# Kernel optimization log

Measured on AMD Instinct MI355X. Metric: run time of the kernel, lower is better.

Reference implementation:

```python
import jax, jax.numpy as jnp
import numpy as np

B, N, C = 2, 4096, 1024
H, WIN = 16, 20
D = C // H

def setup_inputs() -> dict:
    key = jax.random.key(0)
    ks = jax.random.split(key, 9)
    s = 1.0 / np.sqrt(C)
    d = {"q": jax.random.normal(ks[0], (B, N, C), jnp.float32)}
    for i, name in enumerate(["Wq", "Wk", "Wv", "Wo"]):
        d[name + "_w"] = jax.random.normal(ks[1 + 2 * i], (C, C), jnp.float32) * s
        d[name + "_b"] = jax.random.normal(ks[2 + 2 * i], (C,), jnp.float32) * 0.01
    return d

def reference(q, Wq_w, Wq_b, Wk_w, Wk_b, Wv_w, Wv_b, Wo_w, Wo_b):
    b, n, c = q.shape
    w2 = WIN // 2  # half window = 10
    def proj(x, w, bias):
        return (x @ w.T + bias).reshape(b, n, H, D).transpose(0, 2, 1, 3)  # [B,H,N,D]
    Q = proj(q, Wq_w, Wq_b)
    K = proj(q, Wk_w, Wk_b)
    V = proj(q, Wv_w, Wv_b)
    off = jnp.arange(-w2, w2 + 1)                       # [Wn] = 21 offsets
    pos = jnp.arange(n)[:, None] + off[None, :]         # [N, Wn] key index per query
    valid = (pos >= 0) & (pos < n)                      # edge clipping == torch start/end slicing
    idx = jnp.clip(pos, 0, n - 1)
    Kw = K[:, :, idx, :]                                # [B,H,N,Wn,D] gathered key windows
    Vw = V[:, :, idx, :]
    scale = jnp.sqrt(jnp.float32(D))
    scores = jnp.einsum('bhnd,bhnwd->bhnw', Q, Kw) / scale
    scores = jnp.where(valid[None, None], scores, -jnp.inf)
    probs = jax.nn.softmax(scores, axis=-1)             # invalid slots get exactly 0
    out = jnp.einsum('bhnw,bhnwd->bhnd', probs, Vw)
    out = out.transpose(0, 2, 1, 3).reshape(b, n, c)
    out = out @ Wo_w.T + Wo_b
    # torch returns attn_probs of the LAST loop iteration i=N-1: window [N-1-w2, N), size w2+1
    attn_last = probs[:, :, -1:, : w2 + 1]              # [B,H,1,11]
    return (out, attn_last)
```

## Files before the change

kernel.cpp:

```cpp
#include <hip/hip_runtime.h>
#include <hip/hip_bf16.h>

#define Bb 2
#define Nn 4096
#define Cc 1024
#define Hh 16
#define Dd 64
#define Mm (Bb*Nn)
#define W2 10
#define WINSZ 21

typedef __attribute__((ext_vector_type(8))) short  bf16x8s;
typedef __attribute__((ext_vector_type(4))) float  f32x4;
typedef __attribute__((ext_vector_type(4))) unsigned short us4;

#define AS1 __attribute__((address_space(1)))
#define AS3 __attribute__((address_space(3)))

__device__ __forceinline__ unsigned short f2bf(float f) {
  unsigned int u = __float_as_uint(f);
  u += 0x7FFFu + ((u >> 16) & 1u);
  return (unsigned short)(u >> 16);
}
__device__ __forceinline__ float bflo(unsigned int u) { return __uint_as_float(u << 16); }
__device__ __forceinline__ float bfhi(unsigned int u) { return __uint_as_float(u & 0xFFFF0000u); }

__device__ __forceinline__ us4 cvt4(float4 v) {
  us4 o;
  o.x = f2bf(v.x); o.y = f2bf(v.y); o.z = f2bf(v.z); o.w = f2bf(v.w);
  return o;
}

__global__ __launch_bounds__(256) void cvt_all(const float4* __restrict__ q,
                                               const float4* __restrict__ wq,
                                               const float4* __restrict__ wk,
                                               const float4* __restrict__ wv,
                                               const float4* __restrict__ wo,
                                               const float* __restrict__ bq,
                                               const float* __restrict__ bk,
                                               const float* __restrict__ bv,
                                               us4* __restrict__ qb4,
                                               us4* __restrict__ wqkv4,
                                               us4* __restrict__ wo4,
                                               float* __restrict__ bqkv) {
  const int NQ = 2097152, NW = 262144, TOT = NQ + 4 * NW;
  const int gid = blockIdx.x * 256 + threadIdx.x;
  const int stride = gridDim.x * 256;
  for (int i = gid; i < TOT; i += stride) {
    if (i < NQ) {
      qb4[i] = cvt4(q[i]);
    } else {
      int j = i - NQ;
      int r = j >> 18, k = j & (NW - 1);
      if (r == 0)      wqkv4[k]          = cvt4(wq[k]);
      else if (r == 1) wqkv4[NW + k]     = cvt4(wk[k]);
      else if (r == 2) wqkv4[2 * NW + k] = cvt4(wv[k]);
      else             wo4[k]            = cvt4(wo[k]);
    }
  }
  if (gid < 3072) {
    float v = (gid < 1024) ? bq[gid] : (gid < 2048) ? bk[gid - 1024] : bv[gid - 2048];
    bqkv[gid] = v;
  }
}

template<bool OUT_BF16>
__global__ __launch_bounds__(512) void gemm_p3(const unsigned short* __restrict__ A,
                                               const unsigned short* __restrict__ Bm,
                                               const float* __restrict__ bias,
                                               void* __restrict__ Cout,
                                               int N) {
  constexpr int K = 1024, NT = 16, NBM = Mm / 128;
  __shared__ unsigned short lds[3][24576];

  const int tid = threadIdx.x, wid = tid >> 6, lane = tid & 63;
  const int wm = wid >> 2, wn = wid & 3;

  const int nwg = gridDim.x, cpx = nwg >> 3, bid = blockIdx.x;
  const int swz = (bid & 7) * cpx + (bid >> 3);
  const int m0 = (swz % NBM) << 7, n0 = (swz / NBM) << 8;

  const int rbase = wid * 8 + (lane >> 3);
  const int cst = ((lane & 7) ^ (lane >> 3)) * 8;
  const unsigned short* aS0 = A + (size_t)(m0 + rbase) * K + cst;
  const unsigned short* aS1 = A + (size_t)(m0 + 64 + rbase) * K + cst;
  const unsigned short* bS0 = Bm + (size_t)(n0 + rbase) * K + cst;
  const unsigned short* bS1 = Bm + (size_t)(n0 + 64 + rbase) * K + cst;
  const unsigned short* bS2 = Bm + (size_t)(n0 + 128 + rbase) * K + cst;
  const unsigned short* bS3 = Bm + (size_t)(n0 + 192 + rbase) * K + cst;
  const int dA0 = wid * 512, dA1 = 4096 + wid * 512;
  const int dB0 = 8192 + wid * 512, dB1 = 12288 + wid * 512;
  const int dB2 = 16384 + wid * 512, dB3 = 20480 + wid * 512;

#define STG(bf, kt) do {                                                                   \
    const size_t ko = (size_t)(kt) * 64;                                                   \
    __builtin_amdgcn_global_load_lds((AS1 const void*)(aS0 + ko), (AS3 void*)(&lds[bf][dA0]), 16, 0, 0); \
    __builtin_amdgcn_global_load_lds((AS1 const void*)(aS1 + ko), (AS3 void*)(&lds[bf][dA1]), 16, 0, 0); \
    __builtin_amdgcn_global_load_lds((AS1 const void*)(bS0 + ko), (AS3 void*)(&lds[bf][dB0]), 16, 0, 0); \
    __builtin_amdgcn_global_load_lds((AS1 const void*)(bS1 + ko), (AS3 void*)(&lds[bf][dB1]), 16, 0, 0); \
    __builtin_amdgcn_global_load_lds((AS1 const void*)(bS2 + ko), (AS3 void*)(&lds[bf][dB2]), 16, 0, 0); \
    __builtin_amdgcn_global_load_lds((AS1 const void*)(bS3 + ko), (AS3 void*)(&lds[bf][dB3]), 16, 0, 0); \
  } while (0)

  int aoff[2][4], boff[2][4];
#pragma unroll
  for (int kk = 0; kk < 2; ++kk) {
    const int chs = ((kk * 4 + (lane >> 4)) ^ (lane & 7)) * 8;
#pragma unroll
    for (int f = 0; f < 4; ++f) {
      aoff[kk][f] = (wm * 64 + f * 16 + (lane & 15)) * 64 + chs;
      boff[kk][f] = 8192 + (wn * 64 + f * 16 + (lane & 15)) * 64 + chs;
    }
  }

  f32x4 acc[4][4] = {};

  STG(0, 0);
  STG(1, 1);
  asm volatile("s_waitcnt vmcnt(6)" ::: "memory");
  __builtin_amdgcn_sched_barrier(0);
  __builtin_amdgcn_s_barrier();
  __builtin_amdgcn_sched_barrier(0);

  int cur = 0, stg = 2;
  for (int t = 0; t < NT; ++t) {
    if (t + 2 < NT) STG(stg, t + 2);

    const unsigned short* L = &lds[cur][0];
    bf16x8s a[2][4], b[2][4];
#pragma unroll
    for (int kk = 0; kk < 2; ++kk) {
#pragma unroll
      for (int f = 0; f < 4; ++f) {
        a[kk][f] = *(const bf16x8s*)(L + aoff[kk][f]);
        b[kk][f] = *(const bf16x8s*)(L + boff[kk][f]);
      }
    }
    __builtin_amdgcn_s_setprio(1);
#pragma unroll
    for (int kk = 0; kk < 2; ++kk)
#pragma unroll
      for (int fm = 0; fm < 4; ++fm)
#pragma unroll
        for (int fn = 0; fn < 4; ++fn)
          acc[fm][fn] = __builtin_amdgcn_mfma_f32_16x16x32_bf16(a[kk][fm], b[kk][fn], acc[fm][fn], 0, 0, 0);
    __builtin_amdgcn_s_setprio(0);

    if (t + 1 < NT) {
      if (t + 2 < NT) asm volatile("s_waitcnt vmcnt(6)" ::: "memory");
      else            asm volatile("s_waitcnt vmcnt(0)" ::: "memory");
      __builtin_amdgcn_sched_barrier(0);
      __builtin_amdgcn_s_barrier();
      __builtin_amdgcn_sched_barrier(0);
    }
    cur = (cur == 2) ? 0 : cur + 1;
    stg = (stg == 2) ? 0 : stg + 1;
  }
#undef STG

  const int r0 = m0 + wm * 64 + (lane >> 4) * 4;
  const int c0 = n0 + wn * 64 + (lane & 15);
#pragma unroll
  for (int fm = 0; fm < 4; ++fm) {
#pragma unroll
    for (int fn = 0; fn < 4; ++fn) {
      const int col = c0 + fn * 16;
      const float bv = bias[col];
#pragma unroll
      for (int r = 0; r < 4; ++r) {
        const int row = r0 + fm * 16 + r;
        const float v = acc[fm][fn][r] + bv;
        if (OUT_BF16)
          ((unsigned short*)Cout)[(size_t)row * N + col] = f2bf(v);
        else
          ((float*)Cout)[(size_t)row * N + col] = v;
      }
    }
  }
}

#define TN 128
#define KVROWS (TN + 2 * W2)

__global__ void attn_kernel(const unsigned short* __restrict__ QKV,
                            unsigned short* __restrict__ AO,
                            float* __restrict__ attn_last) {
  __shared__ uint4 Kl[KVROWS * 8];
  __shared__ uint4 Vl[KVROWS * 8];

  const int nt = Nn / TN;
  const int bid = blockIdx.x;
  const int tile = bid & (nt - 1);
  const int bh = bid / nt;
  const int h = bh & (Hh - 1), b = bh / Hh;
  const int n0 = tile * TN;
  const int tid = threadIdx.x;

  for (int idx = tid; idx < KVROWS * 8; idx += 256) {
    const int r = idx >> 3, c = idx & 7;
    const int pos = n0 - W2 + r;
    uint4 kv = make_uint4(0, 0, 0, 0), vv = make_uint4(0, 0, 0, 0);
    if (pos >= 0 && pos < Nn) {
      const uint4* row = (const uint4*)(QKV + (size_t)(b * Nn + pos) * 3072);
      kv = row[128 + h * 8 + c];
      vv = row[256 + h * 8 + c];
    }
    const int slot = c ^ (r & 7);
    Kl[r * 8 + slot] = kv;
    Vl[r * 8 + slot] = vv;
  }
  __syncthreads();

  const int row  = tid >> 1;
  const int half = tid & 1;
  const int n = n0 + row;
  const size_t m = (size_t)b * Nn + n;

  const uint4* qrow = (const uint4*)(QKV + m * 3072) + h * 8 + half * 4;
  const uint4 qd0 = qrow[0], qd1 = qrow[1], qd2 = qrow[2], qd3 = qrow[3];

  float p[WINSZ];
#pragma unroll
  for (int w = 0; w < WINSZ; ++w) p[w] = 0.f;

#pragma unroll
  for (int c = 0; c < 4; ++c) {
    const uint4 qv = (c == 0) ? qd0 : (c == 1) ? qd1 : (c == 2) ? qd2 : qd3;
    const float q0 = bflo(qv.x), q1 = bfhi(qv.x);
    const float q2 = bflo(qv.y), q3 = bfhi(qv.y);
    const float q4 = bflo(qv.z), q5 = bfhi(qv.z);
    const float q6 = bflo(qv.w), q7 = bfhi(qv.w);
#pragma unroll 7
    for (int w = 0; w < WINSZ; ++w) {
      const int r = row + w;
      const uint4 v = Kl[r * 8 + ((half * 4 + c) ^ (r & 7))];
      float a0 = q0 * bflo(v.x);
      float a1 = q1 * bfhi(v.x);
      a0 += q2 * bflo(v.y);
      a1 += q3 * bfhi(v.y);
      a0 += q4 * bflo(v.z);
      a1 += q5 * bfhi(v.z);
      a0 += q6 * bflo(v.w);
      a1 += q7 * bfhi(v.w);
      p[w] += a0 + a1;
    }
  }

#pragma unroll
  for (int w = 0; w < WINSZ; ++w) {
    float t = p[w];
    t += __shfl_xor(t, 1, 64);
    const int pos = n - W2 + w;
    p[w] = (pos < 0 || pos >= Nn) ? -1e30f : t * 0.125f;
  }
  float mx = p[0];
#pragma unroll
  for (int w = 1; w < WINSZ; ++w) mx = fmaxf(mx, p[w]);
  float sum = 0.f;
#pragma unroll
  for (int w = 0; w < WINSZ; ++w) { p[w] = __expf(p[w] - mx); sum += p[w]; }
  const float inv = 1.0f / sum;

  if (n == Nn - 1 && half == 0) {
#pragma unroll
    for (int w = 0; w <= W2; ++w)
      attn_last[(b * Hh + h) * (W2 + 1) + w] = p[w] * inv;
  }

  uint4* orow = (uint4*)(AO + m * Cc + h * Dd) + half * 4;
#pragma unroll
  for (int c = 0; c < 4; ++c) {
    float o0 = 0.f, o1 = 0.f, o2 = 0.f, o3 = 0.f;
    float o4 = 0.f, o5 = 0.f, o6 = 0.f, o7 = 0.f;
#pragma unroll 7
    for (int w = 0; w < WINSZ; ++w) {
      const int r = row + w;
      const uint4 v = Vl[r * 8 + ((half * 4 + c) ^ (r & 7))];
      const float pw = p[w];
      o0 += pw * bflo(v.x);
      o1 += pw * bfhi(v.x);
      o2 += pw * bflo(v.y);
      o3 += pw * bfhi(v.y);
      o4 += pw * bflo(v.z);
      o5 += pw * bfhi(v.z);
      o6 += pw * bflo(v.w);
      o7 += pw * bfhi(v.w);
    }
    unsigned int d0 = (unsigned int)f2bf(o0 * inv) | ((unsigned int)f2bf(o1 * inv) << 16);
    unsigned int d1 = (unsigned int)f2bf(o2 * inv) | ((unsigned int)f2bf(o3 * inv) << 16);
    unsigned int d2 = (unsigned int)f2bf(o4 * inv) | ((unsigned int)f2bf(o5 * inv) << 16);
    unsigned int d3 = (unsigned int)f2bf(o6 * inv) | ((unsigned int)f2bf(o7 * inv) << 16);
    orow[c] = make_uint4(d0, d1, d2, d3);
  }
}

extern "C" void kernel_launch(void* const* d_in, const int* in_sizes, int n_in,
                              void* d_out, int out_size, void* d_ws, size_t ws_size,
                              hipStream_t stream) {
  const float* q    = (const float*)d_in[0];
  const float* Wq_w = (const float*)d_in[1];
  const float* Wq_b = (const float*)d_in[2];
  const float* Wk_w = (const float*)d_in[3];
  const float* Wk_b = (const float*)d_in[4];
  const float* Wv_w = (const float*)d_in[5];
  const float* Wv_b = (const float*)d_in[6];
  const float* Wo_w = (const float*)d_in[7];
  const float* Wo_b = (const float*)d_in[8];
  float* out = (float*)d_out;
  float* attn_last = out + (size_t)Mm * Cc;

  char* ws = (char*)d_ws;
  unsigned short* qb   = (unsigned short*)(ws);
  unsigned short* Wqkv = (unsigned short*)(ws + 16777216);
  unsigned short* Wo16 = (unsigned short*)(ws + 16777216 + 6291456);
  float*          bqkv = (float*)(ws + 25165824);
  unsigned short* QKV  = (unsigned short*)(ws + 25182208);
  unsigned short* AO   = (unsigned short*)(ws + 75513856);

  cvt_all<<<2048, 256, 0, stream>>>((const float4*)q,
                                    (const float4*)Wq_w, (const float4*)Wk_w,
                                    (const float4*)Wv_w, (const float4*)Wo_w,
                                    Wq_b, Wk_b, Wv_b,
                                    (us4*)qb, (us4*)Wqkv, (us4*)Wo16, bqkv);

  {
    dim3 grid((Mm / 128) * (3072 / 256));
    gemm_p3<true><<<grid, 512, 0, stream>>>(qb, Wqkv, bqkv, (void*)QKV, 3072);
  }

  {
    dim3 grid(Bb * Hh * (Nn / TN));
    attn_kernel<<<grid, 256, 0, stream>>>(QKV, AO, attn_last);
  }

  {
    dim3 grid((Mm / 128) * (Cc / 256));
    gemm_p3<false><<<grid, 512, 0, stream>>>(AO, Wo16, Wo_b, (void*)out, Cc);
  }
}
```

Measured before the change: 134.5 us.

## Use 256x256-tile GEMM with K-step 32 for QKV projection

Adds a new GEMM kernel with 256x256 output tiles and 32-wide K slices, triple-buffered via global_load_lds, each warp computing 128x64 with 8x4 MFMA fragments. It replaces the 128x256 tile kernel for the QKV projection, raising arithmetic intensity per LDS byte and halving the number of workgroups. In exchange it uses more accumulator registers (128 floats per lane) and has fewer blocks (384) for the CU count, which may hurt occupancy and wave balance.

Measured after the change: 141.1 us. 4.9% more time.

```diff
diff --git a/kernel.cpp b/kernel.cpp
--- a/kernel.cpp
+++ b/kernel.cpp
@@ -65,12 +65,116 @@
 }
 
 template<bool OUT_BF16>
+__global__ __launch_bounds__(512) void gemm_b256(const unsigned short* __restrict__ A,
+                                                 const unsigned short* __restrict__ Bm,
+                                                 const float* __restrict__ bias,
+                                                 void* __restrict__ Cout,
+                                                 int N) {
+  constexpr int K = 1024, NT = 32;
+  __shared__ unsigned short lds[3][16384];
+
+  const int tid = threadIdx.x, wid = tid >> 6, lane = tid & 63;
+  const int wm = wid >> 2, wn = wid & 3;
+
+  const int nwg = gridDim.x, cpx = nwg >> 3, bid = blockIdx.x;
+  const int swz = (bid & 7) * cpx + (bid >> 3);
+  constexpr int NBM = Mm / 256;
+  const int m0 = (swz % NBM) << 8, n0 = (swz / NBM) << 8;
+
+  const int srow = lane >> 2;
+  const int g8 = ((lane & 3) ^ ((lane >> 3) & 3)) * 8;
+  const unsigned short* aS0 = A  + (size_t)(m0 + wid * 32 + srow) * K + g8;
+  const unsigned short* aS1 = aS0 + (size_t)16 * K;
+  const unsigned short* bS0 = Bm + (size_t)(n0 + wid * 32 + srow) * K + g8;
+  const unsigned short* bS1 = bS0 + (size_t)16 * K;
+  const int dA0 = wid * 1024, dA1 = wid * 1024 + 512;
+  const int dB0 = 8192 + wid * 1024, dB1 = 8192 + wid * 1024 + 512;
+
+#define STG(bf, kt) do {                                                                    \
+    const size_t ko = (size_t)(kt) * 32;                                                    \
+    __builtin_amdgcn_global_load_lds((AS1 const void*)(aS0 + ko), (AS3 void*)(&lds[bf][dA0]), 16, 0, 0); \
+    __builtin_amdgcn_global_load_lds((AS1 const void*)(aS1 + ko), (AS3 void*)(&lds[bf][dA1]), 16, 0, 0); \
+    __builtin_amdgcn_global_load_lds((AS1 const void*)(bS0 + ko), (AS3 void*)(&lds[bf][dB0]), 16, 0, 0); \
+    __builtin_amdgcn_global_load_lds((AS1 const void*)(bS1 + ko), (AS3 void*)(&lds[bf][dB1]), 16, 0, 0); \
+  } while (0)
+
+  const int slot8 = ((lane >> 4) ^ (((lane & 15) >> 1) & 3)) * 8;
+  int aoff[8], boff[4];
+#pragma unroll
+  for (int f = 0; f < 8; ++f)
+    aoff[f] = (wm * 128 + f * 16 + (lane & 15)) * 32 + slot8;
+#pragma unroll
+  for (int f = 0; f < 4; ++f)
+    boff[f] = 8192 + (wn * 64 + f * 16 + (lane & 15)) * 32 + slot8;
+
+  f32x4 acc[8][4] = {};
+
+  STG(0, 0);
+  STG(1, 1);
+  asm volatile("s_waitcnt vmcnt(4)" ::: "memory");
+  __builtin_amdgcn_sched_barrier(0);
+  __builtin_amdgcn_s_barrier();
+  __builtin_amdgcn_sched_barrier(0);
+
+  int cur = 0, stg = 2;
+#pragma unroll 1
+  for (int t = 0; t < NT; ++t) {
+    if (t + 2 < NT) STG(stg, t + 2);
+
+    const unsigned short* L = &lds[cur][0];
+    bf16x8s a[8], b[4];
+#pragma unroll
+    for (int f = 0; f < 8; ++f) a[f] = *(const bf16x8s*)(L + aoff[f]);
+#pragma unroll
+    for (int f = 0; f < 4; ++f) b[f] = *(const bf16x8s*)(L + boff[f]);
+    __builtin_amdgcn_s_setprio(1);
+#pragma unroll
+    for (int fm = 0; fm < 8; ++fm)
+#pragma unroll
+      for (int fn = 0; fn < 4; ++fn)
+        acc[fm][fn] = __builtin_amdgcn_mfma_f32_16x16x32_bf16(a[fm], b[fn], acc[fm][fn], 0, 0, 0);
+    __builtin_amdgcn_s_setprio(0);
+
+    if (t + 1 < NT) {
+      if (t + 2 < NT) asm volatile("s_waitcnt vmcnt(4)" ::: "memory");
+      else            asm volatile("s_waitcnt vmcnt(0)" ::: "memory");
+      __builtin_amdgcn_sched_barrier(0);
+      __builtin_amdgcn_s_barrier();
+      __builtin_amdgcn_sched_barrier(0);
+    }
+    cur = (cur == 2) ? 0 : cur + 1;
+    stg = (stg == 2) ? 0 : stg + 1;
+  }
+#undef STG
+
+  const int r0 = m0 + wm * 128 + (lane >> 4) * 4;
+  const int c0 = n0 + wn * 64 + (lane & 15);
+#pragma unroll
+  for (int fm = 0; fm < 8; ++fm) {
+#pragma unroll
+    for (int fn = 0; fn < 4; ++fn) {
+      const int col = c0 + fn * 16;
+      const float bv = bias[col];
+#pragma unroll
+      for (int r = 0; r < 4; ++r) {
+        const int row = r0 + fm * 16 + r;
+        const float v = acc[fm][fn][r] + bv;
+        if (OUT_BF16)
+          ((unsigned short*)Cout)[(size_t)row * N + col] = f2bf(v);
+        else
+          ((float*)Cout)[(size_t)row * N + col] = v;
+      }
+    }
+  }
+}
+
+template<bool OUT_BF16>
 __global__ __launch_bounds__(512) void gemm_p3(const unsigned short* __restrict__ A,
                                                const unsigned short* __restrict__ Bm,
                                                const float* __restrict__ bias,
                                                void* __restrict__ Cout,
                                                int N) {
-  constexpr int K = 1024, NT = 16, NBM = Mm / 128;
+  constexpr int K = 1024, NT = 16;
   __shared__ unsigned short lds[3][24576];
 
   const int tid = threadIdx.x, wid = tid >> 6, lane = tid & 63;
@@ -78,6 +182,7 @@
 
   const int nwg = gridDim.x, cpx = nwg >> 3, bid = blockIdx.x;
   const int swz = (bid & 7) * cpx + (bid >> 3);
+  constexpr int NBM = Mm / 128;
   const int m0 = (swz % NBM) << 7, n0 = (swz / NBM) << 8;
 
   const int rbase = wid * 8 + (lane >> 3);
@@ -324,8 +429,8 @@
                                     (us4*)qb, (us4*)Wqkv, (us4*)Wo16, bqkv);
 
   {
-    dim3 grid((Mm / 128) * (3072 / 256));
-    gemm_p3<true><<<grid, 512, 0, stream>>>(qb, Wqkv, bqkv, (void*)QKV, 3072);
+    dim3 grid((Mm / 256) * (3072 / 256));
+    gemm_b256<true><<<grid, 512, 0, stream>>>(qb, Wqkv, bqkv, (void*)QKV, 3072);
   }
 
   {
```

## Use 256x256-tile ping-pong GEMM with setprio for QKV projection

Applied to the files above, without the earlier changes.

Adds a new GEMM kernel using 256x256 output tiles, double-buffered LDS (128KB), and a phased schedule. In that schedule MFMA blocks are wrapped in s_setprio and interleaved with LDS reads and global_load_lds staging of the next k-tiles. It replaces the 128x256 triple-buffered kernel for the QKV projection only. The larger tile raises data reuse per loaded byte, and the fine-grained interleave aims to overlap loads with math. The cost is more barriers, heavy register use (32 accumulators), and fewer workgroups (384), which may hurt occupancy and tail balance.

Result: slower. 137.5 us (+2.3%).

```diff
diff --git a/kernel.cpp b/kernel.cpp
--- a/kernel.cpp
+++ b/kernel.cpp
@@ -65,12 +65,122 @@
 }
 
 template<bool OUT_BF16>
+__global__ __launch_bounds__(512) void gemm8p(const unsigned short* __restrict__ A,
+                                              const unsigned short* __restrict__ Bm,
+                                              const float* __restrict__ bias,
+                                              void* __restrict__ Cout,
+                                              int N) {
+  constexpr int K = 1024;
+  __shared__ unsigned short lds[65536];
+
+  const int tid = threadIdx.x, wid = tid >> 6, lane = tid & 63;
+  const int wm = wid >> 2, wn = wid & 3;
+
+  const int nwg = gridDim.x, cpx = nwg >> 3, bid = blockIdx.x;
+  const int swz = (bid & 7) * cpx + (bid >> 3);
+  constexpr int NBM = Mm / 256;
+  const int m0 = (swz % NBM) << 8, n0 = (swz / NBM) << 8;
+
+  const int rbase = wid * 8 + (lane >> 3);
+  const int cst = ((lane & 7) ^ (lane >> 3)) * 8;
+  const unsigned short* aP0 = A  + (size_t)(m0 + rbase) * K + cst;
+  const unsigned short* aP1 = aP0 + (size_t)128 * K;
+  const unsigned short* bP0 = Bm + (size_t)(n0 + rbase) * K + cst;
+  const unsigned short* bP1 = bP0 + (size_t)128 * K;
+
+  const int awb = wm * 8192 + (lane & 15) * 64;
+  const int bwb = 16384 + (wn >> 1) * 8192 + (wn & 1) * 4096 + (lane & 15) * 64;
+  const int chs0 = (((lane >> 4)) ^ (lane & 7)) * 8;
+  const int chs1 = ((4 + (lane >> 4)) ^ (lane & 7)) * 8;
+
+  f32x4 acc[8][4] = {};
+  bf16x8s breg[4][2], areg[2][2];
+
+#define GL(sp, off) __builtin_amdgcn_global_load_lds((AS1 const void*)(sp), (AS3 void*)(&lds[off]), 16, 0, 0)
+#define STGA(d,h,kt) do { const unsigned short* _s = ((h) ? aP1 : aP0) + (size_t)(kt) * 64; \
+    GL(_s,                   (d)*32768 + (h)*8192 +        wid*512); \
+    GL(_s + (size_t)64 * K,  (d)*32768 + (h)*8192 + 4096 + wid*512); } while (0)
+#define STGB(d,h,kt) do { const unsigned short* _s = ((h) ? bP1 : bP0) + (size_t)(kt) * 64; \
+    GL(_s,                   (d)*32768 + 16384 + (h)*8192 +        wid*512); \
+    GL(_s + (size_t)64 * K,  (d)*32768 + 16384 + (h)*8192 + 4096 + wid*512); } while (0)
+#define LDB(d) do { _Pragma("unroll") for (int fn = 0; fn < 4; ++fn) { \
+    breg[fn][0] = *(const bf16x8s*)(&lds[(d)*32768 + bwb + fn*1024 + chs0]); \
+    breg[fn][1] = *(const bf16x8s*)(&lds[(d)*32768 + bwb + fn*1024 + chs1]); } } while (0)
+#define LDA(d,q) do { _Pragma("unroll") for (int u = 0; u < 2; ++u) { \
+    areg[u][0] = *(const bf16x8s*)(&lds[(d)*32768 + awb + ((q)*2+u)*1024 + chs0]); \
+    areg[u][1] = *(const bf16x8s*)(&lds[(d)*32768 + awb + ((q)*2+u)*1024 + chs1]); } } while (0)
+#define MF16(q) do { _Pragma("unroll") for (int u = 0; u < 2; ++u) _Pragma("unroll") for (int fn = 0; fn < 4; ++fn) { \
+    acc[(q)*2+u][fn] = __builtin_amdgcn_mfma_f32_16x16x32_bf16(areg[u][0], breg[fn][0], acc[(q)*2+u][fn], 0, 0, 0); \
+    acc[(q)*2+u][fn] = __builtin_amdgcn_mfma_f32_16x16x32_bf16(areg[u][1], breg[fn][1], acc[(q)*2+u][fn], 0, 0, 0); } } while (0)
+#define BAR __builtin_amdgcn_s_barrier()
+#define LGKM0 asm volatile("s_waitcnt lgkmcnt(0)" ::: "memory")
+#define PRIO1 __builtin_amdgcn_s_setprio(1)
+#define PRIO0 __builtin_amdgcn_s_setprio(0)
+
+  STGA(0,0,0); STGA(0,1,0); STGB(0,0,0); STGB(0,1,0);
+  STGA(1,0,1); STGA(1,1,1); STGB(1,0,1); STGB(1,1,1);
+  asm volatile("s_waitcnt vmcnt(8)" ::: "memory");
+  BAR;
+
+#pragma unroll 1
+  for (int j = 0; j < 8; ++j) {
+    const int tA1 = 2*j + 1;
+    const int t0  = (2*j + 2) & 15;
+    const int tB1 = (2*j + 3) & 15;
+    LDB(0); LDA(0,0); STGA(1,0,tA1);          BAR; LGKM0;
+    PRIO1; MF16(0); PRIO0; BAR;
+    LDA(0,1); STGA(1,1,tA1); STGB(0,0,t0);    BAR; LGKM0;
+    PRIO1; MF16(1); PRIO0; BAR;
+    LDA(0,2); STGB(0,1,t0);                   BAR; LGKM0;
+    PRIO1; MF16(2); PRIO0; BAR;
+    LDA(0,3);                                 BAR; LGKM0;
+    PRIO1; MF16(3); PRIO0;
+    asm volatile("s_waitcnt vmcnt(4)" ::: "memory"); BAR;
+    LDB(1); LDA(1,0); STGA(0,0,t0);           BAR; LGKM0;
+    PRIO1; MF16(0); PRIO0; BAR;
+    LDA(1,1); STGA(0,1,t0); STGB(1,0,tB1);    BAR; LGKM0;
+    PRIO1; MF16(1); PRIO0; BAR;
+    LDA(1,2); STGB(1,1,tB1);                  BAR; LGKM0;
+    PRIO1; MF16(2); PRIO0; BAR;
+    LDA(1,3);                                 BAR; LGKM0;
+    PRIO1; MF16(3); PRIO0;
+    asm volatile("s_waitcnt vmcnt(4)" ::: "memory"); BAR;
+  }
+#undef GL
+#undef STGA
+#undef STGB
+#undef LDB
+#undef LDA
+#undef MF16
+
+  const int r0 = m0 + wm * 128 + (lane >> 4) * 4;
+  const int c0 = n0 + wn * 64 + (lane & 15);
+#pragma unroll
+  for (int fm = 0; fm < 8; ++fm) {
+#pragma unroll
+    for (int fn = 0; fn < 4; ++fn) {
+      const int col = c0 + fn * 16;
+      const float bv = bias[col];
+#pragma unroll
+      for (int r = 0; r < 4; ++r) {
+        const int row = r0 + fm * 16 + r;
+        const float v = acc[fm][fn][r] + bv;
+        if (OUT_BF16)
+          ((unsigned short*)Cout)[(size_t)row * N + col] = f2bf(v);
+        else
+          ((float*)Cout)[(size_t)row * N + col] = v;
+      }
+    }
+  }
+}
+
+template<bool OUT_BF16>
 __global__ __launch_bounds__(512) void gemm_p3(const unsigned short* __restrict__ A,
                                                const unsigned short* __restrict__ Bm,
                                                const float* __restrict__ bias,
                                                void* __restrict__ Cout,
                                                int N) {
-  constexpr int K = 1024, NT = 16, NBM = Mm / 128;
+  constexpr int K = 1024, NT = 16;
   __shared__ unsigned short lds[3][24576];
 
   const int tid = threadIdx.x, wid = tid >> 6, lane = tid & 63;
@@ -78,6 +188,7 @@
 
   const int nwg = gridDim.x, cpx = nwg >> 3, bid = blockIdx.x;
   const int swz = (bid & 7) * cpx + (bid >> 3);
+  constexpr int NBM = Mm / 128;
   const int m0 = (swz % NBM) << 7, n0 = (swz / NBM) << 8;
 
   const int rbase = wid * 8 + (lane >> 3);
@@ -324,8 +435,8 @@
                                     (us4*)qb, (us4*)Wqkv, (us4*)Wo16, bqkv);
 
   {
-    dim3 grid((Mm / 128) * (3072 / 256));
-    gemm_p3<true><<<grid, 512, 0, stream>>>(qb, Wqkv, bqkv, (void*)QKV, 3072);
+    dim3 grid((Mm / 256) * (3072 / 256));
+    gemm8p<true><<<grid, 512, 0, stream>>>(qb, Wqkv, bqkv, (void*)QKV, 3072);
   }
 
   {
```

## Load GEMM B operand directly from global into registers, double-buffered

Applied to the files above, without the earlier changes.

The GEMM kernel no longer stages the weight (B) tile through LDS. Each wave loads its own B fragments straight from global memory into a double-buffered register set, prefetching the next k-step while the current one computes. A still goes through the 3-stage LDS ring, whose size drops from 24576 to 8192 shorts per stage, and the vmcnt waits are retuned. The aim is less LDS traffic and footprint and higher occupancy, at the cost of more VGPRs and uncoalesced, redundant global reads of B across the waves that share a column block.

New measurement: 212.7 us. 1.58x slower.

```diff
diff --git a/kernel.cpp b/kernel.cpp
--- a/kernel.cpp
+++ b/kernel.cpp
@@ -65,77 +65,76 @@
 }
 
 template<bool OUT_BF16>
-__global__ __launch_bounds__(512) void gemm_p3(const unsigned short* __restrict__ A,
+__global__ __launch_bounds__(512) void gemm_bd(const unsigned short* __restrict__ A,
                                                const unsigned short* __restrict__ Bm,
                                                const float* __restrict__ bias,
                                                void* __restrict__ Cout,
                                                int N) {
-  constexpr int K = 1024, NT = 16, NBM = Mm / 128;
-  __shared__ unsigned short lds[3][24576];
+  constexpr int K = 1024, NT = 16;
+  __shared__ unsigned short lds[3][8192];
 
   const int tid = threadIdx.x, wid = tid >> 6, lane = tid & 63;
   const int wm = wid >> 2, wn = wid & 3;
 
   const int nwg = gridDim.x, cpx = nwg >> 3, bid = blockIdx.x;
   const int swz = (bid & 7) * cpx + (bid >> 3);
+  constexpr int NBM = Mm / 128;
   const int m0 = (swz % NBM) << 7, n0 = (swz / NBM) << 8;
 
   const int rbase = wid * 8 + (lane >> 3);
   const int cst = ((lane & 7) ^ (lane >> 3)) * 8;
   const unsigned short* aS0 = A + (size_t)(m0 + rbase) * K + cst;
   const unsigned short* aS1 = A + (size_t)(m0 + 64 + rbase) * K + cst;
-  const unsigned short* bS0 = Bm + (size_t)(n0 + rbase) * K + cst;
-  const unsigned short* bS1 = Bm + (size_t)(n0 + 64 + rbase) * K + cst;
-  const unsigned short* bS2 = Bm + (size_t)(n0 + 128 + rbase) * K + cst;
-  const unsigned short* bS3 = Bm + (size_t)(n0 + 192 + rbase) * K + cst;
   const int dA0 = wid * 512, dA1 = 4096 + wid * 512;
-  const int dB0 = 8192 + wid * 512, dB1 = 12288 + wid * 512;
-  const int dB2 = 16384 + wid * 512, dB3 = 20480 + wid * 512;
-
-#define STG(bf, kt) do {                                                                   \
-    const size_t ko = (size_t)(kt) * 64;                                                   \
+
+  const unsigned short* bBase = Bm + (size_t)(n0 + wn * 64 + (lane & 15)) * K + (lane >> 4) * 8;
+
+#define STGA(bf, kt) do { const size_t ko = (size_t)(kt) * 64;                              \
     __builtin_amdgcn_global_load_lds((AS1 const void*)(aS0 + ko), (AS3 void*)(&lds[bf][dA0]), 16, 0, 0); \
     __builtin_amdgcn_global_load_lds((AS1 const void*)(aS1 + ko), (AS3 void*)(&lds[bf][dA1]), 16, 0, 0); \
-    __builtin_amdgcn_global_load_lds((AS1 const void*)(bS0 + ko), (AS3 void*)(&lds[bf][dB0]), 16, 0, 0); \
-    __builtin_amdgcn_global_load_lds((AS1 const void*)(bS1 + ko), (AS3 void*)(&lds[bf][dB1]), 16, 0, 0); \
-    __builtin_amdgcn_global_load_lds((AS1 const void*)(bS2 + ko), (AS3 void*)(&lds[bf][dB2]), 16, 0, 0); \
-    __builtin_amdgcn_global_load_lds((AS1 const void*)(bS3 + ko), (AS3 void*)(&lds[bf][dB3]), 16, 0, 0); \
   } while (0)
 
-  int aoff[2][4], boff[2][4];
+#define BLOAD(dst, kt) do { _Pragma("unroll") for (int i = 0; i < 8; ++i)                   \
+    dst[i] = *(const bf16x8s*)(bBase + (size_t)(i & 3) * 16 * K + (size_t)(kt) * 64 + (i >> 2) * 32); \
+  } while (0)
+
+  int aoff[2][4];
 #pragma unroll
   for (int kk = 0; kk < 2; ++kk) {
     const int chs = ((kk * 4 + (lane >> 4)) ^ (lane & 7)) * 8;
 #pragma unroll
-    for (int f = 0; f < 4; ++f) {
+    for (int f = 0; f < 4; ++f)
       aoff[kk][f] = (wm * 64 + f * 16 + (lane & 15)) * 64 + chs;
-      boff[kk][f] = 8192 + (wn * 64 + f * 16 + (lane & 15)) * 64 + chs;
-    }
   }
 
   f32x4 acc[4][4] = {};
-
-  STG(0, 0);
-  STG(1, 1);
-  asm volatile("s_waitcnt vmcnt(6)" ::: "memory");
+  bf16x8s b0[8], b1[8];
+
+  STGA(0, 0);
+  STGA(1, 1);
+  BLOAD(b0, 0);
+  asm volatile("s_waitcnt vmcnt(10)" ::: "memory");
   __builtin_amdgcn_sched_barrier(0);
   __builtin_amdgcn_s_barrier();
   __builtin_amdgcn_sched_barrier(0);
 
   int cur = 0, stg = 2;
+#pragma unroll 2
   for (int t = 0; t < NT; ++t) {
-    if (t + 2 < NT) STG(stg, t + 2);
+    bf16x8s (&bc)[8] = (t & 1) ? b1 : b0;
+    bf16x8s (&bn)[8] = (t & 1) ? b0 : b1;
+
+    if (t + 2 < NT) STGA(stg, t + 2);
+    if (t + 1 < NT) BLOAD(bn, t + 1);
 
     const unsigned short* L = &lds[cur][0];
-    bf16x8s a[2][4], b[2][4];
-#pragma unroll
-    for (int kk = 0; kk < 2; ++kk) {
-#pragma unroll
-      for (int f = 0; f < 4; ++f) {
+    bf16x8s a[2][4];
+#pragma unroll
+    for (int kk = 0; kk < 2; ++kk)
+#pragma unroll
+      for (int f = 0; f < 4; ++f)
         a[kk][f] = *(const bf16x8s*)(L + aoff[kk][f]);
-        b[kk][f] = *(const bf16x8s*)(L + boff[kk][f]);
-      }
-    }
+
     __builtin_amdgcn_s_setprio(1);
 #pragma unroll
     for (int kk = 0; kk < 2; ++kk)
@@ -143,12 +142,12 @@
       for (int fm = 0; fm < 4; ++fm)
 #pragma unroll
         for (int fn = 0; fn < 4; ++fn)
-          acc[fm][fn] = __builtin_amdgcn_mfma_f32_16x16x32_bf16(a[kk][fm], b[kk][fn], acc[fm][fn], 0, 0, 0);
+          acc[fm][fn] = __builtin_amdgcn_mfma_f32_16x16x32_bf16(a[kk][fm], bc[kk * 4 + fn], acc[fm][fn], 0, 0, 0);
     __builtin_amdgcn_s_setprio(0);
 
     if (t + 1 < NT) {
-      if (t + 2 < NT) asm volatile("s_waitcnt vmcnt(6)" ::: "memory");
-      else            asm volatile("s_waitcnt vmcnt(0)" ::: "memory");
+      if (t + 2 < NT) asm volatile("s_waitcnt vmcnt(10)" ::: "memory");
+      else            asm volatile("s_waitcnt vmcnt(8)"  ::: "memory");
       __builtin_amdgcn_sched_barrier(0);
       __builtin_amdgcn_s_barrier();
       __builtin_amdgcn_sched_barrier(0);
@@ -156,7 +155,8 @@
     cur = (cur == 2) ? 0 : cur + 1;
     stg = (stg == 2) ? 0 : stg + 1;
   }
-#undef STG
+#undef STGA
+#undef BLOAD
 
   const int r0 = m0 + wm * 64 + (lane >> 4) * 4;
   const int c0 = n0 + wn * 64 + (lane & 15);
@@ -325,7 +325,7 @@
 
   {
     dim3 grid((Mm / 128) * (3072 / 256));
-    gemm_p3<true><<<grid, 512, 0, stream>>>(qb, Wqkv, bqkv, (void*)QKV, 3072);
+    gemm_bd<true><<<grid, 512, 0, stream>>>(qb, Wqkv, bqkv, (void*)QKV, 3072);
   }
 
   {
@@ -335,6 +335,6 @@
 
   {
     dim3 grid((Mm / 128) * (Cc / 256));
-    gemm_p3<false><<<grid, 512, 0, stream>>>(AO, Wo16, Wo_b, (void*)out, Cc);
-  }
-}
+    gemm_bd<false><<<grid, 512, 0, stream>>>(AO, Wo16, Wo_b, (void*)out, Cc);
+  }
+}
```
